# Performance work log

Measured on AMD Instinct MI355X. Metric: run time of the kernel, lower is better.

Reference implementation:

```python
import jax, jax.numpy as jnp
import numpy as np

D_MODEL = 4096
N_HEADS = 32
N_KV = 8
HEAD_DIM = D_MODEL // N_HEADS  # 128
GROUP = N_HEADS // N_KV        # 4
BATCH = 2
SEQ = 2048


def _rope_cos_sin(seq_len, head_dim):
    inv_freq = 1.0 / (10000.0 ** (jnp.arange(0, head_dim, 2, dtype=jnp.float32) / head_dim))
    t = jnp.arange(seq_len, dtype=jnp.float32)
    freqs = jnp.outer(t, inv_freq)            # [S, D/2]
    emb = jnp.concatenate([freqs, freqs], -1)  # [S, D]
    return jnp.cos(emb), jnp.sin(emb)


def _rotate_half(x):
    d = x.shape[-1] // 2
    return jnp.concatenate([-x[..., d:], x[..., :d]], axis=-1)


def setup_inputs() -> dict:
    key = jax.random.key(0)
    ks = jax.random.split(key, 5)
    s = 0.02
    x = jax.random.normal(ks[0], (BATCH, SEQ, D_MODEL), jnp.float32)
    Wq = jax.random.normal(ks[1], (D_MODEL, D_MODEL), jnp.float32) * s
    Wk = jax.random.normal(ks[2], (D_MODEL, N_KV * HEAD_DIM), jnp.float32) * s
    Wv = jax.random.normal(ks[3], (D_MODEL, N_KV * HEAD_DIM), jnp.float32) * s
    Wo = jax.random.normal(ks[4], (D_MODEL, D_MODEL), jnp.float32) * s
    # causal mask: True where attention is disallowed (masked_fill semantics)
    mask = jnp.triu(jnp.ones((SEQ, SEQ), jnp.bool_), k=1)
    mask = jnp.broadcast_to(mask, (BATCH, SEQ, SEQ))
    return {"x": x, "mask": mask, "Wq": Wq, "Wk": Wk, "Wv": Wv, "Wo": Wo}


def reference(x, mask, Wq, Wk, Wv, Wo):
    B, S, _ = x.shape
    scaling = HEAD_DIM ** -0.5
    q = (x @ Wq).reshape(B, S, N_HEADS, HEAD_DIM).transpose(0, 2, 1, 3)  # [B,H,S,D]
    k = (x @ Wk).reshape(B, S, N_KV, HEAD_DIM).transpose(0, 2, 1, 3)     # [B,Kv,S,D]
    v = (x @ Wv).reshape(B, S, N_KV, HEAD_DIM).transpose(0, 2, 1, 3)
    cos, sin = _rope_cos_sin(S, HEAD_DIM)  # [S,D]
    cos = cos[None, None]
    sin = sin[None, None]
    q = q * cos + _rotate_half(q) * sin
    k = k * cos + _rotate_half(k) * sin
    # GQA: group queries per kv head instead of repeat_interleave (same math)
    qg = q.reshape(B, N_KV, GROUP, S, HEAD_DIM)
    scores = jnp.einsum('bkgqd,bkld->bkgql', qg, k) * scaling  # [B,Kv,G,S,S]
    scores = jnp.where(mask[:, None, None], -jnp.inf, scores)
    attn = jax.nn.softmax(scores, axis=-1)
    out = jnp.einsum('bkgql,bkld->bkgqd', attn, v)             # [B,Kv,G,S,D]
    out = out.reshape(B, N_HEADS, S, HEAD_DIM).transpose(0, 2, 1, 3).reshape(B, S, D_MODEL)
    return out @ Wo
```

## Files before the change

kernel.cpp:

```cpp
#include <hip/hip_runtime.h>
#include <hip/hip_bf16.h>

typedef __hip_bfloat16 bf16;
typedef float f32x4 __attribute__((ext_vector_type(4)));
typedef short bf16x8 __attribute__((ext_vector_type(8)));
typedef short bf16x4 __attribute__((ext_vector_type(4)));

#define D_MODEL 4096
#define N_HEADS 32
#define N_KV 8
#define HEAD_DIM 128
#define SEQ 2048
#define BATCH 2
#define NTOK (BATCH * SEQ)

static __device__ __forceinline__ float b2f(bf16 v) { return __bfloat162float(v); }
static __device__ __forceinline__ bf16 f2b(float v) { return __float2bfloat16(v); }
static __device__ __forceinline__ short f2bs(float v) {
  union { bf16 b; short s; } u; u.b = f2b(v); return u.s;
}

static __device__ __forceinline__ void async_ld16(const bf16* g, bf16* l) {
  __builtin_amdgcn_global_load_lds(
      (const __attribute__((address_space(1))) void*)g,
      (__attribute__((address_space(3))) void*)l, 16, 0, 0);
}

__global__ __launch_bounds__(256) void cast_f32_to_bf16(const float* __restrict__ in,
                                                        bf16* __restrict__ out, int n4) {
  int i = blockIdx.x * 256 + threadIdx.x;
  if (i >= n4) return;
  float4 v = ((const float4*)in)[i];
  union { ushort4 u; bf16 b[4]; } o;
  o.b[0] = f2b(v.x); o.b[1] = f2b(v.y); o.b[2] = f2b(v.z); o.b[3] = f2b(v.w);
  ((ushort4*)out)[i] = o.u;
}

__global__ __launch_bounds__(256) void transpose_cast(const float* __restrict__ in,
                                                      bf16* __restrict__ out, int R, int C) {
  __shared__ bf16 tile[64][65];
  const int c0 = blockIdx.x * 64;
  const int r0 = blockIdx.y * 64;
  const int t = threadIdx.x;
  const int tc = t & 63, tr = t >> 6;
  for (int i = 0; i < 16; i++) {
    int r = tr + i * 4;
    tile[tc][r] = f2b(in[(size_t)(r0 + r) * C + c0 + tc]);
  }
  __syncthreads();
  for (int i = 0; i < 16; i++) {
    int r = tr + i * 4;
    out[(size_t)(c0 + r) * R + r0 + tc] = tile[r][tc];
  }
}

__global__ __launch_bounds__(256) void transpose_v(const bf16* __restrict__ in,
                                                   bf16* __restrict__ out) {
  __shared__ __align__(16) bf16 tile[64][72];
  const int b = blockIdx.z;
  const int s0 = blockIdx.y * 64, c0 = blockIdx.x * 64;
  const int t = threadIdx.x;
  const int rr = t >> 3, g8 = (t & 7) * 8;
#pragma unroll
  for (int i = 0; i < 2; i++) {
    int s = rr + i * 32;
    *(int4*)&tile[s][g8] = *(const int4*)&in[((size_t)(b * 2048 + s0 + s)) * 1024 + c0 + g8];
  }
  __syncthreads();
#pragma unroll
  for (int i = 0; i < 2; i++) {
    int c = rr + i * 32;
    bf16 tmp[8];
#pragma unroll
    for (int j = 0; j < 8; j++) tmp[j] = tile[g8 + j][c];
    *(int4*)&out[((size_t)(b * 1024 + c0 + c)) * 2048 + s0 + g8] = *(int4*)tmp;
  }
}

static __device__ __forceinline__ void store_out(float* p, float v) { *p = v; }
static __device__ __forceinline__ void store_out(bf16* p, float v) { *p = f2b(v); }

template <typename OutT>
__global__ __launch_bounds__(256) void gemm_bt(const bf16* __restrict__ A,
                                               const bf16* __restrict__ Bt,
                                               OutT* __restrict__ C,
                                               int M, int N, int K) {
  __shared__ __align__(16) bf16 As[128][32];
  __shared__ __align__(16) bf16 Bs[128][32];
  const int t = threadIdx.x;
  const int m0 = blockIdx.y * 128;
  const int n0 = blockIdx.x * 128;
  const int lane = t & 63, wave = t >> 6;
  const int wm = (wave >> 1) * 64, wn = (wave & 1) * 64;
  const int lr = lane & 15, quad = lane >> 4;

  const int srow = wave * 16 + (lane >> 2);
  const int skg = (lane & 3) << 3;
  const bf16* Ap0 = A + (size_t)(m0 + srow) * K + skg;
  const bf16* Ap1 = A + (size_t)(m0 + 64 + srow) * K + skg;
  const bf16* Bp0 = Bt + (size_t)(n0 + srow) * K + skg;
  const bf16* Bp1 = Bt + (size_t)(n0 + 64 + srow) * K + skg;
  bf16* lA0 = &As[wave * 16][0];
  bf16* lA1 = &As[64 + wave * 16][0];
  bf16* lB0 = &Bs[wave * 16][0];
  bf16* lB1 = &Bs[64 + wave * 16][0];

  f32x4 acc[4][4] = {};

  for (int k0 = 0; k0 < K; k0 += 32) {
    async_ld16(Ap0 + k0, lA0);
    async_ld16(Ap1 + k0, lA1);
    async_ld16(Bp0 + k0, lB0);
    async_ld16(Bp1 + k0, lB1);
    __syncthreads();
    bf16x8 a[4], b[4];
#pragma unroll
    for (int i = 0; i < 4; i++) a[i] = *(const bf16x8*)&As[wm + i * 16 + lr][quad * 8];
#pragma unroll
    for (int j = 0; j < 4; j++) b[j] = *(const bf16x8*)&Bs[wn + j * 16 + lr][quad * 8];
#pragma unroll
    for (int i = 0; i < 4; i++)
#pragma unroll
      for (int j = 0; j < 4; j++)
        acc[i][j] = __builtin_amdgcn_mfma_f32_16x16x32_bf16(a[i], b[j], acc[i][j], 0, 0, 0);
    __syncthreads();
  }
#pragma unroll
  for (int i = 0; i < 4; i++) {
    int row = m0 + wm + i * 16 + quad * 4;
#pragma unroll
    for (int j = 0; j < 4; j++) {
      int col = n0 + wn + j * 16 + lr;
#pragma unroll
      for (int r = 0; r < 4; r++)
        store_out(&C[(size_t)(row + r) * N + col], acc[i][j][r]);
    }
  }
}

static __device__ __forceinline__ void stage_half(const bf16* __restrict__ base, int r0,
                                                  int kt, int h, bf16* lds_half,
                                                  int wid, int lane) {
#pragma unroll
  for (int rd = 0; rd < 2; rd++) {
    int G = rd * 512 + wid * 64 + lane;
    int r = G >> 3, gr = G & 7;
    int gs = gr ^ (r & 7);
    async_ld16(base + (size_t)(r0 + h * 128 + r) * 4096 + kt * 64 + gs * 8,
               lds_half + (rd * 512 + wid * 64) * 8);
  }
}

template <typename OutT>
__global__ __launch_bounds__(512, 2) void gemm256(const bf16* __restrict__ A,
                                                  const bf16* __restrict__ Bt,
                                                  OutT* __restrict__ C,
                                                  int M, int N) {
  __shared__ __align__(16) bf16 As[2][256][64];
  __shared__ __align__(16) bf16 Bs[2][256][64];
  const int t = threadIdx.x, lane = t & 63, wid = t >> 6;
  const int lr = lane & 15, quad = lane >> 4;
  const int wm = wid >> 2, wn = wid & 3;

  const int nbx = N >> 8;
  int bid = blockIdx.x;
  int swz = (bid & 7) * ((int)gridDim.x >> 3) + (bid >> 3);
  const int m0 = (swz / nbx) * 256, n0 = (swz % nbx) * 256;

#define A_FRAG(buf, mi, ks)                                                       \
  (*(const bf16x8*)&As[buf][((mi) >> 2) * 128 + wm * 64 + ((mi) & 3) * 16 + lr]   \
        [((((ks) << 2) | quad) ^ (lr & 7)) << 3])
#define B_FRAG(buf, ni, ks)                                                       \
  (*(const bf16x8*)&Bs[buf][((ni) >> 1) * 128 + wn * 32 + ((ni) & 1) * 16 + lr]   \
        [((((ks) << 2) | quad) ^ (lr & 7)) << 3])

  f32x4 acc[8][4] = {};
  bf16x8 areg[4][2], b0[2][2], b1[2][2];
  const int NT = 4096 / 64;

  stage_half(A,  m0, 0, 0, &As[0][0][0],   wid, lane);
  stage_half(Bt, n0, 0, 0, &Bs[0][0][0],   wid, lane);
  stage_half(A,  m0, 0, 1, &As[0][128][0], wid, lane);
  stage_half(Bt, n0, 0, 1, &Bs[0][128][0], wid, lane);
  stage_half(A,  m0, 1, 0, &As[1][0][0],   wid, lane);
  stage_half(Bt, n0, 1, 0, &Bs[1][0][0],   wid, lane);
  asm volatile("s_waitcnt vmcnt(4)" ::: "memory");
  __builtin_amdgcn_s_barrier();

  for (int s = 0; s < NT; s++) {
    const int buf = s & 1, nb = buf ^ 1;

#pragma unroll
    for (int mi = 0; mi < 4; mi++)
#pragma unroll
      for (int ks = 0; ks < 2; ks++) areg[mi][ks] = A_FRAG(buf, mi, ks);
#pragma unroll
    for (int ni = 0; ni < 2; ni++)
#pragma unroll
      for (int ks = 0; ks < 2; ks++) b0[ni][ks] = B_FRAG(buf, ni, ks);
    if (s + 1 < NT) stage_half(A, m0, s + 1, 1, &As[nb][128][0], wid, lane);
    __builtin_amdgcn_s_barrier();
    __builtin_amdgcn_s_setprio(1);
#pragma unroll
    for (int mi = 0; mi < 4; mi++)
#pragma unroll
      for (int ni = 0; ni < 2; ni++)
#pragma unroll
        for (int ks = 0; ks < 2; ks++)
          acc[mi][ni] = __builtin_amdgcn_mfma_f32_16x16x32_bf16(areg[mi][ks], b0[ni][ks],
                                                                acc[mi][ni], 0, 0, 0);
    __builtin_amdgcn_s_setprio(0);
    __builtin_amdgcn_s_barrier();

#pragma unroll
    for (int ni = 0; ni < 2; ni++)
#pragma unroll
      for (int ks = 0; ks < 2; ks++) b1[ni][ks] = B_FRAG(buf, ni + 2, ks);
    if (s + 1 < NT) stage_half(Bt, n0, s + 1, 1, &Bs[nb][128][0], wid, lane);
    __builtin_amdgcn_s_barrier();
    __builtin_amdgcn_s_setprio(1);
#pragma unroll
    for (int mi = 0; mi < 4; mi++)
#pragma unroll
      for (int ni = 0; ni < 2; ni++)
#pragma unroll
        for (int ks = 0; ks < 2; ks++)
          acc[mi][ni + 2] = __builtin_amdgcn_mfma_f32_16x16x32_bf16(areg[mi][ks], b1[ni][ks],
                                                                    acc[mi][ni + 2], 0, 0, 0);
    __builtin_amdgcn_s_setprio(0);
    __builtin_amdgcn_s_barrier();

#pragma unroll
    for (int mi = 0; mi < 4; mi++)
#pragma unroll
      for (int ks = 0; ks < 2; ks++) areg[mi][ks] = A_FRAG(buf, mi + 4, ks);
    if (s + 2 < NT) stage_half(A, m0, s + 2, 0, &As[buf][0][0], wid, lane);
    __builtin_amdgcn_s_barrier();
    __builtin_amdgcn_s_setprio(1);
#pragma unroll
    for (int mi = 0; mi < 4; mi++)
#pragma unroll
      for (int ni = 0; ni < 2; ni++)
#pragma unroll
        for (int ks = 0; ks < 2; ks++)
          acc[mi + 4][ni] = __builtin_amdgcn_mfma_f32_16x16x32_bf16(areg[mi][ks], b0[ni][ks],
                                                                    acc[mi + 4][ni], 0, 0, 0);
    __builtin_amdgcn_s_setprio(0);
    __builtin_amdgcn_s_barrier();

    if (s + 2 < NT) stage_half(Bt, n0, s + 2, 0, &Bs[buf][0][0], wid, lane);
    __builtin_amdgcn_s_barrier();
    __builtin_amdgcn_s_setprio(1);
#pragma unroll
    for (int mi = 0; mi < 4; mi++)
#pragma unroll
      for (int ni = 0; ni < 2; ni++)
#pragma unroll
        for (int ks = 0; ks < 2; ks++)
          acc[mi + 4][ni + 2] = __builtin_amdgcn_mfma_f32_16x16x32_bf16(areg[mi][ks], b1[ni][ks],
                                                                        acc[mi + 4][ni + 2], 0, 0, 0);
    __builtin_amdgcn_s_setprio(0);
    if (s + 2 < NT) {
      asm volatile("s_waitcnt vmcnt(4)" ::: "memory");
    } else if (s + 1 < NT) {
      asm volatile("s_waitcnt vmcnt(0)" ::: "memory");
    }
    __builtin_amdgcn_s_barrier();
  }
#undef A_FRAG
#undef B_FRAG

#pragma unroll
  for (int mi = 0; mi < 8; mi++) {
    int row = m0 + (mi >> 2) * 128 + wm * 64 + (mi & 3) * 16 + quad * 4;
#pragma unroll
    for (int ni = 0; ni < 4; ni++) {
      int col = n0 + (ni >> 1) * 128 + wn * 32 + (ni & 1) * 16 + lr;
#pragma unroll
      for (int r = 0; r < 4; r++)
        store_out(&C[(size_t)(row + r) * N + col], acc[mi][ni][r]);
    }
  }
}

__global__ __launch_bounds__(256) void rope_kernel(bf16* __restrict__ X, int lh, float scale) {
  int idx = blockIdx.x * 256 + threadIdx.x;
  int d = idx & 63;
  int rest = idx >> 6;
  int h = rest & ((1 << lh) - 1);
  int tok = rest >> lh;
  float ang = (float)(tok & (SEQ - 1)) * exp2f((float)d * -0.2076205059304602f);
  float sn, cs;
  sincosf(ang, &sn, &cs);
  bf16* p = X + (((size_t)tok << lh) + h) * HEAD_DIM + d;
  float x0 = b2f(p[0]), x1 = b2f(p[64]);
  p[0]  = f2b((x0 * cs - x1 * sn) * scale);
  p[64] = f2b((x1 * cs + x0 * sn) * scale);
}

static __device__ __forceinline__ void stage_kv(const bf16* kbase, const bf16* vtbase,
                                                bf16* ksb, bf16* vtb,
                                                int jt, int w, int lane) {
#pragma unroll
  for (int rd = 0; rd < 2; rd++) {
    int G = rd * 512 + w * 64 + lane;
    int r = G >> 4;
    int gs = (G & 15) ^ (r & 7);
    async_ld16(kbase + (size_t)(jt * 64 + r) * 1024 + gs * 8, ksb + (rd * 512 + w * 64) * 8);
  }
#pragma unroll
  for (int rd = 0; rd < 2; rd++) {
    int G = rd * 512 + w * 64 + lane;
    int d = G >> 3;
    int gs = (G & 7) ^ (d & 7);
    async_ld16(vtbase + (size_t)d * 2048 + jt * 64 + gs * 8, vtb + (rd * 512 + w * 64) * 8);
  }
}

__global__ __launch_bounds__(512) void flash_attn(const bf16* __restrict__ Q,
                                                  const bf16* __restrict__ K,
                                                  const bf16* __restrict__ VT,
                                                  bf16* __restrict__ O) {
  __shared__ __align__(16) bf16 Ks[2][64][128];
  __shared__ __align__(16) bf16 Vt[2][128][64];

  const int qb = (int)gridDim.x - 1 - (int)blockIdx.x;
  const int h = blockIdx.y, b = blockIdx.z;
  const int kvh = h >> 2;
  const int t = threadIdx.x, lane = t & 63, w = t >> 6;
  const int lr = lane & 15, quad = lane >> 4;

  const bf16* kbase = K + ((size_t)(b * SEQ) * N_KV + kvh) * HEAD_DIM;
  const bf16* vtbase = VT + (size_t)(b * 1024 + kvh * 128) * 2048;

  int koff[4], voff[4];
#pragma unroll
  for (int ks = 0; ks < 4; ks++) koff[ks] = (((ks << 2) + quad) ^ (lr & 7)) << 3;
#pragma unroll
  for (int j = 0; j < 4; j++)
    voff[j] = (((((j << 1) + (quad >> 1)) ^ (lr & 7)) << 3) + ((quad & 1) << 2));

  const int tok = b * SEQ + qb * 128 + w * 16 + lr;

  bf16x8 qf[4];
  {
    const bf16* qrow = Q + (size_t)tok * D_MODEL + h * HEAD_DIM + quad * 8;
#pragma unroll
    for (int ks = 0; ks < 4; ks++) qf[ks] = *(const bf16x8*)(qrow + ks * 32);
  }

  f32x4 o_acc[8] = {};
  float m_i = -1e30f, l_i = 0.f;

  const int nt = 2 * qb + 2;
  bf16* ksc = &Ks[0][0][0]; bf16* vtc = &Vt[0][0][0];
  bf16* ksn = &Ks[1][0][0]; bf16* vtn = &Vt[1][0][0];

  stage_kv(kbase, vtbase, ksc, vtc, 0, w, lane);
  __syncthreads();

  for (int jt = 0; jt < nt; jt++) {
    if (jt + 1 < nt) stage_kv(kbase, vtbase, ksn, vtn, jt + 1, w, lane);

    if (jt * 64 <= qb * 128 + w * 16 + 15) {
      f32x4 s_acc[4] = {};
#pragma unroll
      for (int j = 0; j < 4; j++) {
        const bf16* krow = ksc + (j * 16 + lr) * 128;
#pragma unroll
        for (int ks = 0; ks < 4; ks++) {
          bf16x8 kf = *(const bf16x8*)(krow + koff[ks]);
          s_acc[j] = __builtin_amdgcn_mfma_f32_16x16x32_bf16(kf, qf[ks], s_acc[j], 0, 0, 0);
        }
      }

      if (jt >= 2 * qb) {
        int sq = w * 16 + lr;
        int kb0 = jt * 64 - qb * 128;
#pragma unroll
        for (int j = 0; j < 4; j++)
#pragma unroll
          for (int r = 0; r < 4; r++)
            if (kb0 + j * 16 + quad * 4 + r > sq) s_acc[j][r] = -1e30f;
      }

      float mx = -1e30f;
#pragma unroll
      for (int j = 0; j < 4; j++)
#pragma unroll
        for (int r = 0; r < 4; r++) mx = fmaxf(mx, s_acc[j][r]);
      mx = fmaxf(mx, __shfl_xor(mx, 16));
      mx = fmaxf(mx, __shfl_xor(mx, 32));
      float mnew = fmaxf(m_i, mx);
      float alpha = exp2f(m_i - mnew);
      m_i = mnew;

      float p[4][4];
      float sum = 0.f;
#pragma unroll
      for (int j = 0; j < 4; j++)
#pragma unroll
        for (int r = 0; r < 4; r++) {
          p[j][r] = exp2f(s_acc[j][r] - mnew);
          sum += p[j][r];
        }
      sum += __shfl_xor(sum, 16);
      sum += __shfl_xor(sum, 32);
      l_i = l_i * alpha + sum;

#pragma unroll
      for (int n = 0; n < 8; n++)
#pragma unroll
        for (int r = 0; r < 4; r++) o_acc[n][r] *= alpha;

      bf16x4 pf[4];
#pragma unroll
      for (int j = 0; j < 4; j++) {
        pf[j][0] = f2bs(p[j][0]); pf[j][1] = f2bs(p[j][1]);
        pf[j][2] = f2bs(p[j][2]); pf[j][3] = f2bs(p[j][3]);
      }

#pragma unroll
      for (int j = 0; j < 4; j++)
#pragma unroll
        for (int n = 0; n < 8; n++) {
          bf16x4 vf = *(const bf16x4*)(vtc + (n * 16 + lr) * 64 + voff[j]);
          o_acc[n] = __builtin_amdgcn_mfma_f32_16x16x16bf16_1k(vf, pf[j], o_acc[n], 0, 0, 0);
        }
    }

    __syncthreads();
    bf16* tp;
    tp = ksc; ksc = ksn; ksn = tp;
    tp = vtc; vtc = vtn; vtn = tp;
  }

  {
    float inv_l = 1.f / l_i;
    bf16* obase = O + (size_t)tok * D_MODEL + h * HEAD_DIM + quad * 4;
#pragma unroll
    for (int n = 0; n < 8; n++) {
      bf16x4 ov;
      ov[0] = f2bs(o_acc[n][0] * inv_l); ov[1] = f2bs(o_acc[n][1] * inv_l);
      ov[2] = f2bs(o_acc[n][2] * inv_l); ov[3] = f2bs(o_acc[n][3] * inv_l);
      *(bf16x4*)(obase + n * 16) = ov;
    }
  }
}

extern "C" void kernel_launch(void* const* d_in, const int* in_sizes, int n_in,
                              void* d_out, int out_size, void* d_ws, size_t ws_size,
                              hipStream_t stream) {
  const float* x  = (const float*)d_in[0];
  const float* Wq = (const float*)d_in[2];
  const float* Wk = (const float*)d_in[3];
  const float* Wv = (const float*)d_in[4];
  const float* Wo = (const float*)d_in[5];
  float* out = (float*)d_out;

  char* ws = (char*)d_ws;
  const size_t MB = 1024 * 1024;
  bf16* xb  = (bf16*)(ws + 0);
  bf16* WqT = (bf16*)(ws + 32 * MB);
  bf16* WkT = (bf16*)(ws + 64 * MB);
  bf16* WvT = (bf16*)(ws + 72 * MB);
  bf16* WoT = (bf16*)(ws + 80 * MB);
  bf16* Qb  = (bf16*)(ws + 112 * MB);
  bf16* Kb  = (bf16*)(ws + 144 * MB);
  bf16* Vb  = (bf16*)(ws + 152 * MB);
  bf16* VTb = (bf16*)(ws + 160 * MB);
  bf16* Ob  = WqT;

  cast_f32_to_bf16<<<dim3(NTOK * D_MODEL / 4 / 256), 256, 0, stream>>>(x, xb, NTOK * D_MODEL / 4);
  transpose_cast<<<dim3(D_MODEL / 64, D_MODEL / 64), 256, 0, stream>>>(Wq, WqT, D_MODEL, D_MODEL);
  transpose_cast<<<dim3(1024 / 64, D_MODEL / 64), 256, 0, stream>>>(Wk, WkT, D_MODEL, 1024);
  transpose_cast<<<dim3(1024 / 64, D_MODEL / 64), 256, 0, stream>>>(Wv, WvT, D_MODEL, 1024);
  transpose_cast<<<dim3(D_MODEL / 64, D_MODEL / 64), 256, 0, stream>>>(Wo, WoT, D_MODEL, D_MODEL);
  gemm256<bf16><<<dim3(256), 512, 0, stream>>>(xb, WqT, Qb, NTOK, D_MODEL);
  gemm_bt<bf16><<<dim3(1024 / 128, NTOK / 128), 256, 0, stream>>>(xb, WkT, Kb, NTOK, 1024, D_MODEL);
  gemm_bt<bf16><<<dim3(1024 / 128, NTOK / 128), 256, 0, stream>>>(xb, WvT, Vb, NTOK, 1024, D_MODEL);
  rope_kernel<<<dim3(NTOK * N_HEADS * 64 / 256), 256, 0, stream>>>(Qb, 5, 0.12751741737890f);
  rope_kernel<<<dim3(NTOK * N_KV * 64 / 256), 256, 0, stream>>>(Kb, 3, 1.0f);
  transpose_v<<<dim3(1024 / 64, SEQ / 64, BATCH), 256, 0, stream>>>(Vb, VTb);
  flash_attn<<<dim3(SEQ / 128, N_HEADS, BATCH), 512, 0, stream>>>(Qb, Kb, VTb, Ob);
  gemm256<float><<<dim3(256), 512, 0, stream>>>(Ob, WoT, out, NTOK, D_MODEL);
}
```

Measured before the change: 914.6 us.

## Fuse K/V projections into one GEMM, add lazy softmax rescale and MFMA priority

K and V weight matrices are packed side by side so one GEMM with N=2048 writes an interleaved KV buffer. The rope, transpose and attention kernels are changed to read with the new row stride. In flash attention, the running-max update and the rescaling of the output accumulator are skipped unless some row's max grows by more than 8 (in log2 units), saving exp and multiply work. s_setprio is raised around the MFMA blocks. The fused GEMM cuts a launch and gives a larger grid, while the lazy rescale risks larger intermediate values but stays exact after the final normalization.

Result: faster. 822.1 us (-10.1%).

```diff
diff --git a/kernel.cpp b/kernel.cpp
--- a/kernel.cpp
+++ b/kernel.cpp
@@ -13,6 +13,7 @@
 #define SEQ 2048
 #define BATCH 2
 #define NTOK (BATCH * SEQ)
+#define KVSTRIDE 2048
 
 static __device__ __forceinline__ float b2f(bf16 v) { return __bfloat162float(v); }
 static __device__ __forceinline__ bf16 f2b(float v) { return __float2bfloat16(v); }
@@ -64,7 +65,8 @@
 #pragma unroll
   for (int i = 0; i < 2; i++) {
     int s = rr + i * 32;
-    *(int4*)&tile[s][g8] = *(const int4*)&in[((size_t)(b * 2048 + s0 + s)) * 1024 + c0 + g8];
+    *(int4*)&tile[s][g8] =
+        *(const int4*)&in[((size_t)(b * 2048 + s0 + s)) * KVSTRIDE + 1024 + c0 + g8];
   }
   __syncthreads();
 #pragma unroll
@@ -283,7 +285,8 @@
   }
 }
 
-__global__ __launch_bounds__(256) void rope_kernel(bf16* __restrict__ X, int lh, float scale) {
+__global__ __launch_bounds__(256) void rope_kernel(bf16* __restrict__ X, int lh, int lrs,
+                                                   float scale) {
   int idx = blockIdx.x * 256 + threadIdx.x;
   int d = idx & 63;
   int rest = idx >> 6;
@@ -292,7 +295,7 @@
   float ang = (float)(tok & (SEQ - 1)) * exp2f((float)d * -0.2076205059304602f);
   float sn, cs;
   sincosf(ang, &sn, &cs);
-  bf16* p = X + (((size_t)tok << lh) + h) * HEAD_DIM + d;
+  bf16* p = X + ((size_t)tok << lrs) + (h << 7) + d;
   float x0 = b2f(p[0]), x1 = b2f(p[64]);
   p[0]  = f2b((x0 * cs - x1 * sn) * scale);
   p[64] = f2b((x1 * cs + x0 * sn) * scale);
@@ -306,7 +309,8 @@
     int G = rd * 512 + w * 64 + lane;
     int r = G >> 4;
     int gs = (G & 15) ^ (r & 7);
-    async_ld16(kbase + (size_t)(jt * 64 + r) * 1024 + gs * 8, ksb + (rd * 512 + w * 64) * 8);
+    async_ld16(kbase + (size_t)(jt * 64 + r) * KVSTRIDE + gs * 8,
+               ksb + (rd * 512 + w * 64) * 8);
   }
 #pragma unroll
   for (int rd = 0; rd < 2; rd++) {
@@ -318,7 +322,7 @@
 }
 
 __global__ __launch_bounds__(512) void flash_attn(const bf16* __restrict__ Q,
-                                                  const bf16* __restrict__ K,
+                                                  const bf16* __restrict__ KV,
                                                   const bf16* __restrict__ VT,
                                                   bf16* __restrict__ O) {
   __shared__ __align__(16) bf16 Ks[2][64][128];
@@ -330,7 +334,7 @@
   const int t = threadIdx.x, lane = t & 63, w = t >> 6;
   const int lr = lane & 15, quad = lane >> 4;
 
-  const bf16* kbase = K + ((size_t)(b * SEQ) * N_KV + kvh) * HEAD_DIM;
+  const bf16* kbase = KV + (size_t)(b * SEQ) * KVSTRIDE + kvh * HEAD_DIM;
   const bf16* vtbase = VT + (size_t)(b * 1024 + kvh * 128) * 2048;
 
   int koff[4], voff[4];
@@ -364,6 +368,7 @@
 
     if (jt * 64 <= qb * 128 + w * 16 + 15) {
       f32x4 s_acc[4] = {};
+      __builtin_amdgcn_s_setprio(1);
 #pragma unroll
       for (int j = 0; j < 4; j++) {
         const bf16* krow = ksc + (j * 16 + lr) * 128;
@@ -373,6 +378,7 @@
           s_acc[j] = __builtin_amdgcn_mfma_f32_16x16x32_bf16(kf, qf[ks], s_acc[j], 0, 0, 0);
         }
       }
+      __builtin_amdgcn_s_setprio(0);
 
       if (jt >= 2 * qb) {
         int sq = w * 16 + lr;
@@ -391,9 +397,17 @@
         for (int r = 0; r < 4; r++) mx = fmaxf(mx, s_acc[j][r]);
       mx = fmaxf(mx, __shfl_xor(mx, 16));
       mx = fmaxf(mx, __shfl_xor(mx, 32));
-      float mnew = fmaxf(m_i, mx);
-      float alpha = exp2f(m_i - mnew);
-      m_i = mnew;
+
+      if (!__all(mx <= m_i + 8.f)) {
+        float mnew = fmaxf(m_i, mx);
+        float alpha = exp2f(m_i - mnew);
+        m_i = mnew;
+        l_i *= alpha;
+#pragma unroll
+        for (int n = 0; n < 8; n++)
+#pragma unroll
+          for (int r = 0; r < 4; r++) o_acc[n][r] *= alpha;
+      }
 
       float p[4][4];
       float sum = 0.f;
@@ -401,17 +415,12 @@
       for (int j = 0; j < 4; j++)
 #pragma unroll
         for (int r = 0; r < 4; r++) {
-          p[j][r] = exp2f(s_acc[j][r] - mnew);
+          p[j][r] = exp2f(s_acc[j][r] - m_i);
           sum += p[j][r];
         }
       sum += __shfl_xor(sum, 16);
       sum += __shfl_xor(sum, 32);
-      l_i = l_i * alpha + sum;
-
-#pragma unroll
-      for (int n = 0; n < 8; n++)
-#pragma unroll
-        for (int r = 0; r < 4; r++) o_acc[n][r] *= alpha;
+      l_i += sum;
 
       bf16x4 pf[4];
 #pragma unroll
@@ -420,6 +429,7 @@
         pf[j][2] = f2bs(p[j][2]); pf[j][3] = f2bs(p[j][3]);
       }
 
+      __builtin_amdgcn_s_setprio(1);
 #pragma unroll
       for (int j = 0; j < 4; j++)
 #pragma unroll
@@ -427,6 +437,7 @@
           bf16x4 vf = *(const bf16x4*)(vtc + (n * 16 + lr) * 64 + voff[j]);
           o_acc[n] = __builtin_amdgcn_mfma_f32_16x16x16bf16_1k(vf, pf[j], o_acc[n], 0, 0, 0);
         }
+      __builtin_amdgcn_s_setprio(0);
     }
 
     __syncthreads();
@@ -460,28 +471,25 @@
 
   char* ws = (char*)d_ws;
   const size_t MB = 1024 * 1024;
-  bf16* xb  = (bf16*)(ws + 0);
-  bf16* WqT = (bf16*)(ws + 32 * MB);
-  bf16* WkT = (bf16*)(ws + 64 * MB);
-  bf16* WvT = (bf16*)(ws + 72 * MB);
-  bf16* WoT = (bf16*)(ws + 80 * MB);
-  bf16* Qb  = (bf16*)(ws + 112 * MB);
-  bf16* Kb  = (bf16*)(ws + 144 * MB);
-  bf16* Vb  = (bf16*)(ws + 152 * MB);
-  bf16* VTb = (bf16*)(ws + 160 * MB);
-  bf16* Ob  = WqT;
+  bf16* xb   = (bf16*)(ws + 0);
+  bf16* WqT  = (bf16*)(ws + 32 * MB);
+  bf16* WkvT = (bf16*)(ws + 64 * MB);
+  bf16* WoT  = (bf16*)(ws + 80 * MB);
+  bf16* Qb   = (bf16*)(ws + 112 * MB);
+  bf16* KVb  = (bf16*)(ws + 144 * MB);
+  bf16* VTb  = (bf16*)(ws + 160 * MB);
+  bf16* Ob   = WqT;
 
   cast_f32_to_bf16<<<dim3(NTOK * D_MODEL / 4 / 256), 256, 0, stream>>>(x, xb, NTOK * D_MODEL / 4);
   transpose_cast<<<dim3(D_MODEL / 64, D_MODEL / 64), 256, 0, stream>>>(Wq, WqT, D_MODEL, D_MODEL);
-  transpose_cast<<<dim3(1024 / 64, D_MODEL / 64), 256, 0, stream>>>(Wk, WkT, D_MODEL, 1024);
-  transpose_cast<<<dim3(1024 / 64, D_MODEL / 64), 256, 0, stream>>>(Wv, WvT, D_MODEL, 1024);
+  transpose_cast<<<dim3(1024 / 64, D_MODEL / 64), 256, 0, stream>>>(Wk, WkvT, D_MODEL, 1024);
+  transpose_cast<<<dim3(1024 / 64, D_MODEL / 64), 256, 0, stream>>>(Wv, WkvT + (size_t)1024 * 4096, D_MODEL, 1024);
   transpose_cast<<<dim3(D_MODEL / 64, D_MODEL / 64), 256, 0, stream>>>(Wo, WoT, D_MODEL, D_MODEL);
   gemm256<bf16><<<dim3(256), 512, 0, stream>>>(xb, WqT, Qb, NTOK, D_MODEL);
-  gemm_bt<bf16><<<dim3(1024 / 128, NTOK / 128), 256, 0, stream>>>(xb, WkT, Kb, NTOK, 1024, D_MODEL);
-  gemm_bt<bf16><<<dim3(1024 / 128, NTOK / 128), 256, 0, stream>>>(xb, WvT, Vb, NTOK, 1024, D_MODEL);
-  rope_kernel<<<dim3(NTOK * N_HEADS * 64 / 256), 256, 0, stream>>>(Qb, 5, 0.12751741737890f);
-  rope_kernel<<<dim3(NTOK * N_KV * 64 / 256), 256, 0, stream>>>(Kb, 3, 1.0f);
-  transpose_v<<<dim3(1024 / 64, SEQ / 64, BATCH), 256, 0, stream>>>(Vb, VTb);
-  flash_attn<<<dim3(SEQ / 128, N_HEADS, BATCH), 512, 0, stream>>>(Qb, Kb, VTb, Ob);
+  gemm_bt<bf16><<<dim3(KVSTRIDE / 128, NTOK / 128), 256, 0, stream>>>(xb, WkvT, KVb, NTOK, KVSTRIDE, D_MODEL);
+  rope_kernel<<<dim3(NTOK * N_HEADS * 64 / 256), 256, 0, stream>>>(Qb, 5, 12, 0.12751741737890f);
+  rope_kernel<<<dim3(NTOK * N_KV * 64 / 256), 256, 0, stream>>>(KVb, 3, 11, 1.0f);
+  transpose_v<<<dim3(1024 / 64, SEQ / 64, BATCH), 256, 0, stream>>>(KVb, VTb);
+  flash_attn<<<dim3(SEQ / 128, N_HEADS, BATCH), 512, 0, stream>>>(Qb, KVb, VTb, Ob);
   gemm256<float><<<dim3(256), 512, 0, stream>>>(Ob, WoT, out, NTOK, D_MODEL);
 }
```
